# Kernel optimization log

Hardware: AMD Instinct MI355X
Metric: run time of the kernel (lower is better)

The kernel has to match this reference:

```python
import jax, jax.numpy as jnp
import numpy as np

N_NODES = 100000
N_EDGES = 1600000
R_DIM = 8      # radial_embedding_dim (j)
L_DIM = 4      # angular dim (l)
C_DIM = 8      # channel_dim (k)
CUTOFF = 5.5
MP_NORM_FACTOR = 1.0


def setup_inputs() -> dict:
    key = jax.random.key(0)
    k1, k2, k3, k4, k5, k6, k7 = jax.random.split(key, 7)
    node_feat = jax.random.normal(k1, (N_NODES, R_DIM, L_DIM, C_DIM), dtype=jnp.float32)
    edge_lengths = jax.random.uniform(k2, (N_EDGES,), dtype=jnp.float32) * CUTOFF
    radial_cutoff_fn = jax.random.uniform(k3, (N_EDGES,), dtype=jnp.float32)
    edge_index = jax.random.randint(k4, (2, N_EDGES), 0, N_NODES, dtype=jnp.int64)
    prefactor = jax.random.uniform(k5, (R_DIM, C_DIM), dtype=jnp.float32)
    invr0 = (jax.random.uniform(k6, (R_DIM, C_DIM), dtype=jnp.float32) + 0.5) / CUTOFF
    memory_coef = jnp.float32(0.25)
    return {
        "node_feat": node_feat,
        "edge_lengths": edge_lengths,
        "radial_cutoff_fn": radial_cutoff_fn,
        "edge_index": edge_index,
        "prefactor": prefactor,
        "invr0": invr0,
        "memory_coef": memory_coef,
    }


def reference(node_feat, edge_lengths, radial_cutoff_fn, edge_index, prefactor, invr0, memory_coef):
    n_nodes = node_feat.shape[0]
    # radial decay: [E, R, C] = exp(-len * invr0) * prefactor * cutoff_fn
    radial_decay = (
        jnp.exp(-edge_lengths[:, None, None] * invr0)
        * prefactor
        * radial_cutoff_fn[:, None, None]
    )
    # gather sender features [E, R, L, C] and modulate per (edge, radial, channel)
    sender = node_feat[edge_index[0]]
    message = sender * radial_decay[:, :, None, :]
    # scatter-sum messages to receiver nodes
    agg = jax.ops.segment_sum(message, edge_index[1], num_segments=n_nodes)
    return node_feat * memory_coef + agg * MP_NORM_FACTOR
```

## Files before the change

### kernel.cpp

```cpp
#include <hip/hip_runtime.h>
#include <hip/hip_fp16.h>

#define RLC 256
#define BUCKET 32
#define OVF_CAP 65536
#define SCAN_BLOCK 256
#define SCAN_ITEMS 4

__device__ __forceinline__ float fast_exp2(float x) {
#if __has_builtin(__builtin_amdgcn_exp2f)
    return __builtin_amdgcn_exp2f(x);
#else
    return __expf(x * 0.6931471805599453f);
#endif
}

__device__ __forceinline__ unsigned int bfr(float f) {
    unsigned int u = __float_as_uint(f);
    return (u + 0x7fffu + ((u >> 16) & 1u)) >> 16;
}

#define LOG2E 1.4426950408889634f


__global__ __launch_bounds__(256) void build_cast_kernel(
    const int* __restrict__ edge_index,
    const float* __restrict__ edge_len,
    const float* __restrict__ cutoff_fn,
    int* __restrict__ counts,
    int2* __restrict__ payload,
    int4* __restrict__ ovf,
    int* __restrict__ ovf_cnt,
    int n_edges,
    const float4* __restrict__ nf_in,
    uint2* __restrict__ nfbT,
    int nr,
    int nb_build)
{
    if ((int)blockIdx.x < nb_build) {
        int e = blockIdx.x * 256 + threadIdx.x;
        if (e >= n_edges) return;
        int dst = __builtin_nontemporal_load(edge_index + n_edges + e);
        int src = __builtin_nontemporal_load(edge_index + e);
        float  el = __builtin_nontemporal_load(edge_len + e);
        float  cf = __builtin_nontemporal_load(cutoff_fn + e);
        unsigned int hnl = __half_as_ushort(__float2half(-el));
        unsigned int hcf = __half_as_ushort(__float2half(cf));
        unsigned int pk = (hcf << 16) | hnl;
        int r = atomicAdd(&counts[dst], 1);
        if (r < BUCKET) {
            payload[(size_t)dst * BUCKET + r] = make_int2(src, (int)pk);
        } else {
            int o = atomicAdd(ovf_cnt, 1);
            if (o < OVF_CAP) ovf[o] = make_int4(dst, src, (int)pk, 0);
        }
    } else {
        int i = (blockIdx.x - nb_build) * 256 + threadIdx.x;
        if (i >= nr) return;
        const float4* p = nf_in + (size_t)i * 8;
        float v[32];
        #pragma unroll
        for (int q = 0; q < 8; ++q) {
            float4 t = p[q];
            v[4*q+0] = t.x; v[4*q+1] = t.y; v[4*q+2] = t.z; v[4*q+3] = t.w;
        }
        uint2* o = nfbT + (size_t)i * 8;
        #pragma unroll
        for (int c = 0; c < 8; ++c) {
            unsigned int lo = bfr(v[0*8+c]) | (bfr(v[1*8+c]) << 16);
            unsigned int hi = bfr(v[2*8+c]) | (bfr(v[3*8+c]) << 16);
            o[c] = make_uint2(lo, hi);
        }
    }
}

__global__ __launch_bounds__(256) void gather_bucket_kernel(
    const float* __restrict__ node_feat,
    const unsigned short* __restrict__ nfbT,
    const int2* __restrict__ payload,
    const float* __restrict__ prefactor,
    const float* __restrict__ invr0,
    const float* __restrict__ coef_p,
    const int* __restrict__ counts,
    float* __restrict__ out,
    int n_nodes)
{
    int wave = threadIdx.x >> 6;
    int lane = threadIdx.x & 63;
    int node = blockIdx.x * 4 + wave;
    if (node >= n_nodes) return;

    float iv = invr0[lane] * LOG2E;
    float pf = prefactor[lane];
    float coef = *coef_p;

    int r = lane >> 3, c = lane & 7;
    long obase = (long)node * RLC + r * 32 + c;

    int deg = counts[node];
    int m = deg < BUCKET ? deg : BUCKET;

    float a0 = __builtin_nontemporal_load(node_feat + obase)      * coef;
    float a1 = __builtin_nontemporal_load(node_feat + obase + 8)  * coef;
    float a2 = __builtin_nontemporal_load(node_feat + obase + 16) * coef;
    float a3 = __builtin_nontemporal_load(node_feat + obase + 24) * coef;

    const int2* pp = payload + (size_t)node * BUCKET;
    const unsigned short* tb = nfbT + lane * 4;

    #pragma unroll 4
    for (int it = 0; it < m; ++it) {
        int2 p = pp[it];
        int src = p.x;
        unsigned int pk = (unsigned int)p.y;
        float nl = __half2float(__ushort_as_half((unsigned short)(pk & 0xffff)));
        float cf = __half2float(__ushort_as_half((unsigned short)(pk >> 16)));
        float w = fast_exp2(nl * iv) * pf * cf;
        uint2 raw = *(const uint2*)(tb + (size_t)src * RLC);
        float f0 = __uint_as_float(raw.x << 16);
        float f1 = __uint_as_float(raw.x & 0xffff0000u);
        float f2 = __uint_as_float(raw.y << 16);
        float f3 = __uint_as_float(raw.y & 0xffff0000u);
        a0 += w * f0; a1 += w * f1; a2 += w * f2; a3 += w * f3;
    }

    __builtin_nontemporal_store(a0, out + obase);
    __builtin_nontemporal_store(a1, out + obase + 8);
    __builtin_nontemporal_store(a2, out + obase + 16);
    __builtin_nontemporal_store(a3, out + obase + 24);
}

__global__ __launch_bounds__(256) void ovf_kernel(
    const unsigned short* __restrict__ nfbT,
    const float* __restrict__ prefactor,
    const float* __restrict__ invr0,
    const int4* __restrict__ ovf,
    const int* __restrict__ ovf_cnt,
    float* __restrict__ out)
{
    int gtid = blockIdx.x * blockDim.x + threadIdx.x;
    int wid  = gtid >> 6;
    int lane = gtid & 63;
    int nwaves = (gridDim.x * blockDim.x) >> 6;
    int n = *ovf_cnt;
    if (n > OVF_CAP) n = OVF_CAP;

    float iv = invr0[lane] * LOG2E;
    float pf = prefactor[lane];
    int r = lane >> 3, c = lane & 7;

    for (int i = wid; i < n; i += nwaves) {
        int4 rec = ovf[i];
        int dst = rec.x, src = rec.y, pk = rec.z;
        float nl = __half2float(__ushort_as_half((unsigned short)(pk & 0xffff)));
        float cf = __half2float(__ushort_as_half((unsigned short)(((unsigned int)pk) >> 16)));
        float w = fast_exp2(nl * iv) * pf * cf;
        uint2 raw = *(const uint2*)(nfbT + (size_t)src * RLC + lane * 4);
        float f0 = __uint_as_float(raw.x << 16);
        float f1 = __uint_as_float(raw.x & 0xffff0000u);
        float f2 = __uint_as_float(raw.y << 16);
        float f3 = __uint_as_float(raw.y & 0xffff0000u);
        float* o = out + (long)dst * RLC + r * 32 + c;
        atomicAdd(o,      w * f0);
        atomicAdd(o + 8,  w * f1);
        atomicAdd(o + 16, w * f2);
        atomicAdd(o + 24, w * f3);
    }
}


__global__ __launch_bounds__(256) void cast_kernel(
    const float4* __restrict__ in, uint4* __restrict__ outp, int n8)
{
    int i = blockIdx.x * blockDim.x + threadIdx.x;
    if (i >= n8) return;
    float4 a = in[2 * i];
    float4 b = in[2 * i + 1];
    uint4 r;
    r.x = bfr(a.x) | (bfr(a.y) << 16);
    r.y = bfr(a.z) | (bfr(a.w) << 16);
    r.z = bfr(b.x) | (bfr(b.y) << 16);
    r.w = bfr(b.z) | (bfr(b.w) << 16);
    outp[i] = r;
}

__global__ __launch_bounds__(256) void hist_rank_kernel(
    const int* __restrict__ edge_index, int* __restrict__ counts,
    unsigned char* __restrict__ rank, int n_edges)
{
    int e = blockIdx.x * blockDim.x + threadIdx.x;
    if (e >= n_edges) return;
    int dst = edge_index[n_edges + e];
    int r = atomicAdd(&counts[dst], 1);
    rank[e] = (unsigned char)r;
}

__global__ __launch_bounds__(SCAN_BLOCK) void scan1_kernel(
    const int* __restrict__ in, int* __restrict__ out,
    int* __restrict__ blocksums, int n)
{
    __shared__ int tmp[SCAN_BLOCK];
    int t = threadIdx.x;
    int base = blockIdx.x * SCAN_BLOCK * SCAN_ITEMS + t * SCAN_ITEMS;
    int v[SCAN_ITEMS];
    int tot = 0;
    #pragma unroll
    for (int k = 0; k < SCAN_ITEMS; ++k) {
        int i = base + k;
        v[k] = (i < n) ? in[i] : 0;
        tot += v[k];
    }
    tmp[t] = tot;
    __syncthreads();
    int run = tot;
    for (int d = 1; d < SCAN_BLOCK; d <<= 1) {
        int x = (t >= d) ? tmp[t - d] : 0;
        __syncthreads();
        tmp[t] += x;
        __syncthreads();
    }
    int excl = tmp[t] - run;
    #pragma unroll
    for (int k = 0; k < SCAN_ITEMS; ++k) {
        int i = base + k;
        if (i < n) out[i] = excl;
        excl += v[k];
    }
    if (t == SCAN_BLOCK - 1) blocksums[blockIdx.x] = tmp[t];
}

__global__ __launch_bounds__(SCAN_BLOCK) void scan2_kernel(
    int* __restrict__ blocksums, int nb)
{
    __shared__ int tmp[SCAN_BLOCK];
    int t = threadIdx.x;
    int v = (t < nb) ? blocksums[t] : 0;
    tmp[t] = v;
    __syncthreads();
    for (int d = 1; d < SCAN_BLOCK; d <<= 1) {
        int x = (t >= d) ? tmp[t - d] : 0;
        __syncthreads();
        tmp[t] += x;
        __syncthreads();
    }
    if (t < nb) blocksums[t] = tmp[t] - v;
}

__global__ __launch_bounds__(256) void scan3_kernel(
    int* __restrict__ offsets, const int* __restrict__ blocksums,
    int n, int n_edges)
{
    int i = blockIdx.x * blockDim.x + threadIdx.x;
    if (i == 0) offsets[n] = n_edges;
    if (i >= n) return;
    offsets[i] += blocksums[i / (SCAN_BLOCK * SCAN_ITEMS)];
}

__global__ __launch_bounds__(256) void scatter_rank_kernel(
    const int* __restrict__ edge_index,
    const float* __restrict__ edge_len,
    const float* __restrict__ cutoff_fn,
    const int* __restrict__ offsets,
    const unsigned char* __restrict__ rank,
    int2* __restrict__ payload, int n_edges)
{
    int e = blockIdx.x * blockDim.x + threadIdx.x;
    if (e >= n_edges) return;
    int dst = edge_index[n_edges + e];
    int src = edge_index[e];
    unsigned int hnl = __half_as_ushort(__float2half(-edge_len[e]));
    unsigned int hcf = __half_as_ushort(__float2half(cutoff_fn[e]));
    int pos = offsets[dst] + (int)rank[e];
    payload[pos] = make_int2(src, (int)((hcf << 16) | hnl));
}

__global__ __launch_bounds__(256) void gather_kernel(
    const float* __restrict__ node_feat,
    const unsigned short* __restrict__ nfb,
    const int2* __restrict__ payload,
    const float* __restrict__ prefactor,
    const float* __restrict__ invr0,
    const float* __restrict__ coef_p,
    const int*  __restrict__ offsets,
    float* __restrict__ out,
    int n_nodes)
{
    int tid  = blockIdx.x * blockDim.x + threadIdx.x;
    int node = tid >> 6;
    int lane = threadIdx.x & 63;
    if (node >= n_nodes) return;

    int f0     = lane << 2;
    int rcbase = ((f0 >> 5) << 3) + (f0 & 7);

    float4 iv = *(const float4*)(invr0 + rcbase);
    iv.x *= LOG2E; iv.y *= LOG2E; iv.z *= LOG2E; iv.w *= LOG2E;
    const float4 pf = *(const float4*)(prefactor + rcbase);
    float coef = *coef_p;

    const float4 self = *(const float4*)(node_feat + (long)node * RLC + f0);
    float ax = self.x * coef, ay = self.y * coef,
          az = self.z * coef, aw = self.w * coef;

    int j   = offsets[node];
    int end = offsets[node + 1];

    for (int base = j; base < end; base += 64) {
        int idx = base + lane;
        int2 p = make_int2(0, 0);
        if (idx < end) p = payload[idx];
        int m = end - base;
        if (m > 64) m = 64;
        int psrc = p.x;
        int ppk  = p.y;

        #pragma unroll 4
        for (int it = 0; it < m; ++it) {
            int src = __shfl(psrc, it, 64);
            int pk  = __shfl(ppk,  it, 64);
            float nl = __half2float(__ushort_as_half((unsigned short)(pk & 0xffff)));
            float cf = __half2float(__ushort_as_half((unsigned short)(((unsigned int)pk) >> 16)));
            uint2 raw = *(const uint2*)(nfb + (long)src * RLC + f0);
            float fx = __uint_as_float(raw.x << 16);
            float fy = __uint_as_float(raw.x & 0xffff0000u);
            float fz = __uint_as_float(raw.y << 16);
            float fw = __uint_as_float(raw.y & 0xffff0000u);
            ax += fx * (fast_exp2(nl * iv.x) * pf.x * cf);
            ay += fy * (fast_exp2(nl * iv.y) * pf.y * cf);
            az += fz * (fast_exp2(nl * iv.z) * pf.z * cf);
            aw += fw * (fast_exp2(nl * iv.w) * pf.w * cf);
        }
    }

    *(float4*)(out + (long)node * RLC + f0) = make_float4(ax, ay, az, aw);
}

__global__ __launch_bounds__(256) void init_out_kernel(
    const float4* __restrict__ nf4, float4* __restrict__ out4,
    const float* __restrict__ coef_p, int n4)
{
    int i = blockIdx.x * blockDim.x + threadIdx.x;
    if (i >= n4) return;
    float c = *coef_p;
    float4 v = nf4[i];
    out4[i] = make_float4(v.x * c, v.y * c, v.z * c, v.w * c);
}

__global__ __launch_bounds__(256) void edge_scatter_kernel(
    const float* __restrict__ node_feat,
    const float* __restrict__ edge_len,
    const float* __restrict__ cutoff_fn,
    const int*  __restrict__ edge_index,
    const float* __restrict__ prefactor,
    const float* __restrict__ invr0,
    float* __restrict__ out, int n_edges)
{
    int tid  = blockIdx.x * blockDim.x + threadIdx.x;
    int e    = tid >> 6;
    int lane = threadIdx.x & 63;
    if (e >= n_edges) return;
    int   src = edge_index[e];
    int   dst = edge_index[n_edges + e];
    float len = edge_len[e];
    float cf  = cutoff_fn[e];
    int f0     = lane << 2;
    int rcbase = ((f0 >> 5) << 3) + (f0 & 7);
    const float4 iv = *(const float4*)(invr0 + rcbase);
    const float4 pf = *(const float4*)(prefactor + rcbase);
    const float4 s  = *(const float4*)(node_feat + (long)src * RLC + f0);
    float nl = -len;
    float* o = out + (long)dst * RLC + f0;
    atomicAdd(o + 0, s.x * __expf(nl * iv.x) * pf.x * cf);
    atomicAdd(o + 1, s.y * __expf(nl * iv.y) * pf.y * cf);
    atomicAdd(o + 2, s.z * __expf(nl * iv.z) * pf.z * cf);
    atomicAdd(o + 3, s.w * __expf(nl * iv.w) * pf.w * cf);
}

extern "C" void kernel_launch(void* const* d_in, const int* in_sizes, int n_in,
                              void* d_out, int out_size, void* d_ws, size_t ws_size,
                              hipStream_t stream) {
    const float* node_feat  = (const float*)d_in[0];
    const float* edge_len   = (const float*)d_in[1];
    const float* cutoff_fn  = (const float*)d_in[2];
    const int*   edge_index = (const int*)d_in[3];
    const float* prefactor  = (const float*)d_in[4];
    const float* invr0      = (const float*)d_in[5];
    const float* coef_p     = (const float*)d_in[6];
    float* out = (float*)d_out;

    const int n_edges = in_sizes[1];
    const int n_feat  = in_sizes[0];
    const int n_nodes = n_feat / RLC;

    size_t need1 = (size_t)n_feat * 2
                 + (size_t)n_nodes * BUCKET * 8
                 + (size_t)OVF_CAP * 16
                 + (size_t)(n_nodes + 1) * 4;

    const int per_block = SCAN_BLOCK * SCAN_ITEMS;
    const int nb1 = (n_nodes + per_block - 1) / per_block;
    size_t need2 = (size_t)n_feat * 2
                 + (size_t)n_edges * 8
                 + ((size_t)(n_nodes + 1) + n_nodes + 256) * 4
                 + (size_t)n_edges;

    if (ws_size >= need1) {
        unsigned short* nfbT = (unsigned short*)d_ws;
        int2* payload = (int2*)(nfbT + n_feat);
        int4* ovf     = (int4*)(payload + (size_t)n_nodes * BUCKET);
        int*  counts  = (int*)(ovf + OVF_CAP);
        int*  ovf_cnt = counts + n_nodes;

        (void)hipMemsetAsync(counts, 0, (size_t)(n_nodes + 1) * sizeof(int), stream);

        int nr = n_nodes * 8;
        int nb_build = (n_edges + 255) / 256;
        int nb_cast  = (nr + 255) / 256;
        build_cast_kernel<<<nb_build + nb_cast, 256, 0, stream>>>(
            edge_index, edge_len, cutoff_fn, counts, payload, ovf, ovf_cnt,
            n_edges, (const float4*)node_feat, (uint2*)nfbT, nr, nb_build);

        int gg = (n_nodes + 3) / 4;
        gather_bucket_kernel<<<gg, 256, 0, stream>>>(
            node_feat, nfbT, payload, prefactor, invr0, coef_p, counts,
            out, n_nodes);

        ovf_kernel<<<64, 256, 0, stream>>>(
            nfbT, prefactor, invr0, ovf, ovf_cnt, out);
    } else if (ws_size >= need2 && nb1 <= SCAN_BLOCK) {
        unsigned short* nfb = (unsigned short*)d_ws;
        int2* payload   = (int2*)(nfb + n_feat);
        int* offsets    = (int*)(payload + n_edges);
        int* counts     = offsets + (n_nodes + 1);
        int* blocksums  = counts + n_nodes;
        unsigned char* rank = (unsigned char*)(blocksums + 256);

        int n8 = n_feat / 8;
        cast_kernel<<<(n8 + 255) / 256, 256, 0, stream>>>(
            (const float4*)node_feat, (uint4*)nfb, n8);

        (void)hipMemsetAsync(counts, 0, (size_t)n_nodes * sizeof(int), stream);

        int eg = (n_edges + 255) / 256;
        hist_rank_kernel<<<eg, 256, 0, stream>>>(edge_index, counts, rank, n_edges);
        scan1_kernel<<<nb1, SCAN_BLOCK, 0, stream>>>(counts, offsets, blocksums, n_nodes);
        scan2_kernel<<<1, SCAN_BLOCK, 0, stream>>>(blocksums, nb1);
        int ng = (n_nodes + 255) / 256;
        scan3_kernel<<<ng, 256, 0, stream>>>(offsets, blocksums, n_nodes, n_edges);
        scatter_rank_kernel<<<eg, 256, 0, stream>>>(
            edge_index, edge_len, cutoff_fn, offsets, rank, payload, n_edges);

        long total = (long)n_nodes * 64;
        int gg = (int)((total + 255) / 256);
        gather_kernel<<<gg, 256, 0, stream>>>(
            node_feat, nfb, payload, prefactor, invr0, coef_p, offsets,
            out, n_nodes);
    } else {
        int n4 = n_feat / 4;
        init_out_kernel<<<(n4 + 255) / 256, 256, 0, stream>>>(
            (const float4*)node_feat, (float4*)out, coef_p, n4);
        long total_threads = (long)n_edges * 64;
        int grid = (int)((total_threads + 255) / 256);
        edge_scatter_kernel<<<grid, 256, 0, stream>>>(
            node_feat, edge_len, cutoff_fn, edge_index,
            prefactor, invr0, out, n_edges);
    }
}
```

Before: 451.3 us.

## Partition bucket build by destination range per XCD for L2-local atomics

The edge bucketing phase is split into 8 destination-node partitions, interleaved by block index so that each XCD handles one range of receiver nodes. Each block reads the destination indices for 4 edges per thread as a vector and only processes edges whose destination falls in its partition. The aim is to keep the atomics on the counts array and the payload writes inside one XCD's L2 instead of bouncing lines across dies. In exchange, every destination index is read eight times, and the block-to-XCD round-robin mapping the scheme relies on is assumed rather than guaranteed.

```diff
diff --git a/kernel.cpp b/kernel.cpp
--- a/kernel.cpp
+++ b/kernel.cpp
@@ -4,6 +4,7 @@
 #define RLC 256
 #define BUCKET 32
 #define OVF_CAP 65536
+#define NXCD 8
 #define SCAN_BLOCK 256
 #define SCAN_ITEMS 4
 
@@ -35,24 +36,45 @@
     const float4* __restrict__ nf_in,
     uint2* __restrict__ nfbT,
     int nr,
-    int nb_build)
+    int nb_build,
+    int n_nodes)
 {
     if ((int)blockIdx.x < nb_build) {
-        int e = blockIdx.x * 256 + threadIdx.x;
-        if (e >= n_edges) return;
-        int dst = __builtin_nontemporal_load(edge_index + n_edges + e);
-        int src = __builtin_nontemporal_load(edge_index + e);
-        float  el = __builtin_nontemporal_load(edge_len + e);
-        float  cf = __builtin_nontemporal_load(cutoff_fn + e);
-        unsigned int hnl = __half_as_ushort(__float2half(-el));
-        unsigned int hcf = __half_as_ushort(__float2half(cf));
-        unsigned int pk = (hcf << 16) | hnl;
-        int r = atomicAdd(&counts[dst], 1);
-        if (r < BUCKET) {
-            payload[(size_t)dst * BUCKET + r] = make_int2(src, (int)pk);
+        int part  = blockIdx.x & (NXCD - 1);
+        int chunk = blockIdx.x >> 3;
+        int base  = (chunk * 256 + threadIdx.x) * 4;
+        if (base >= n_edges) return;
+        int plo = (int)((long)part * n_nodes / NXCD);
+        int phi = (int)((long)(part + 1) * n_nodes / NXCD);
+
+        int d[4];
+        if (base + 4 <= n_edges) {
+            int4 dv = *(const int4*)(edge_index + n_edges + base);
+            d[0] = dv.x; d[1] = dv.y; d[2] = dv.z; d[3] = dv.w;
         } else {
-            int o = atomicAdd(ovf_cnt, 1);
-            if (o < OVF_CAP) ovf[o] = make_int4(dst, src, (int)pk, 0);
+            #pragma unroll
+            for (int k = 0; k < 4; ++k)
+                d[k] = (base + k < n_edges) ? edge_index[n_edges + base + k] : -1;
+        }
+
+        #pragma unroll
+        for (int k = 0; k < 4; ++k) {
+            int dst = d[k];
+            if (dst < plo || dst >= phi) continue;
+            int e = base + k;
+            int src  = edge_index[e];
+            float el = edge_len[e];
+            float cf = cutoff_fn[e];
+            unsigned int hnl = __half_as_ushort(__float2half(-el));
+            unsigned int hcf = __half_as_ushort(__float2half(cf));
+            unsigned int pk = (hcf << 16) | hnl;
+            int r = atomicAdd(&counts[dst], 1);
+            if (r < BUCKET) {
+                payload[(size_t)dst * BUCKET + r] = make_int2(src, (int)pk);
+            } else {
+                int o = atomicAdd(ovf_cnt, 1);
+                if (o < OVF_CAP) ovf[o] = make_int4(dst, src, (int)pk, 0);
+            }
         }
     } else {
         int i = (blockIdx.x - nb_build) * 256 + threadIdx.x;
@@ -414,11 +436,12 @@
         (void)hipMemsetAsync(counts, 0, (size_t)(n_nodes + 1) * sizeof(int), stream);
 
         int nr = n_nodes * 8;
-        int nb_build = (n_edges + 255) / 256;
+        int nb_build = NXCD * ((n_edges + 1023) / 1024);
         int nb_cast  = (nr + 255) / 256;
         build_cast_kernel<<<nb_build + nb_cast, 256, 0, stream>>>(
             edge_index, edge_len, cutoff_fn, counts, payload, ovf, ovf_cnt,
-            n_edges, (const float4*)node_feat, (uint2*)nfbT, nr, nb_build);
+            n_edges, (const float4*)node_feat, (uint2*)nfbT, nr, nb_build,
+            n_nodes);
 
         int gg = (n_nodes + 3) / 4;
         gather_bucket_kernel<<<gg, 256, 0, stream>>>(
```

After: 429.3 us. 1.05x faster.
